# Kernel tuning notes

Hardware: AMD Instinct MI355X
Metric: run time of the kernel (lower is better)

Reference implementation:

```python
import jax, jax.numpy as jnp
import numpy as np
from jax import lax

R = 512          # num RoIs
K = 81           # num classes (COCO + bg)
IM_H, IM_W = 800, 1333
WX, WY, WW, WH = 10.0, 10.0, 5.0, 5.0   # cfg.MODEL.BBOX_REG_WEIGHTS
XFORM_CLIP = float(np.log(1000.0 / 16.0))  # cfg.BBOX_XFORM_CLIP
NMS_THRESH = 0.5
SCORE_THRESH = 0.001
MAX_PER_IMG = 100
POST_NMS_TOPN = 300


def setup_inputs() -> dict:
    key = jax.random.key(0)
    k1, k2, k3, k4, k5, k6 = jax.random.split(key, 6)
    # Build valid RoIs inside the image (x1<x2, y1<y2)
    cx = jax.random.uniform(k1, (R,)) * IM_W
    cy = jax.random.uniform(k2, (R,)) * IM_H
    w = jax.random.uniform(k3, (R,)) * 200.0 + 20.0
    h = jax.random.uniform(k4, (R,)) * 200.0 + 20.0
    rois = jnp.stack([
        jnp.clip(cx - 0.5 * w, 0.0, IM_W - 1),
        jnp.clip(cy - 0.5 * h, 0.0, IM_H - 1),
        jnp.clip(cx + 0.5 * w, 0.0, IM_W - 1),
        jnp.clip(cy + 0.5 * h, 0.0, IM_H - 1),
    ], axis=1).astype(jnp.float32)
    deltas = (jax.random.normal(k5, (R, 4 * K)) * 0.3).astype(jnp.float32)
    scores = jax.nn.softmax(jax.random.normal(k6, (R, K)) * 2.0, axis=1).astype(jnp.float32)
    return {"rois": rois, "deltas": deltas, "scores": scores}


def bbox_transform(boxes, deltas):
    # boxes [R,4], deltas [R,4K] -> pred boxes [R,K,4], clamped to image
    widths = boxes[:, 2] - boxes[:, 0] + 1.0
    heights = boxes[:, 3] - boxes[:, 1] + 1.0
    ctr_x = boxes[:, 0] + 0.5 * widths
    ctr_y = boxes[:, 1] + 0.5 * heights
    d = deltas.reshape(-1, K, 4)  # [R,K,4]
    dx = d[:, :, 0] / WX
    dy = d[:, :, 1] / WY
    dw = jnp.minimum(d[:, :, 2] / WW, XFORM_CLIP)
    dh = jnp.minimum(d[:, :, 3] / WH, XFORM_CLIP)
    pcx = dx * widths[:, None] + ctr_x[:, None]
    pcy = dy * heights[:, None] + ctr_y[:, None]
    pw = jnp.exp(dw) * widths[:, None]
    ph = jnp.exp(dh) * heights[:, None]
    x1 = jnp.clip(pcx - 0.5 * pw, 0.0, IM_W - 1)
    y1 = jnp.clip(pcy - 0.5 * ph, 0.0, IM_H - 1)
    x2 = jnp.clip(pcx + 0.5 * pw - 1.0, 0.0, IM_W - 1)
    y2 = jnp.clip(pcy + 0.5 * ph - 1.0, 0.0, IM_H - 1)
    return jnp.stack([x1, y1, x2, y2], axis=-1)  # [R,K,4]


def nms_one_class(scores_c, boxes_c):
    # Greedy NMS for one class. scores_c [R], boxes_c [R,4] -> keep mask [R] (orig order)
    order = jnp.argsort(-scores_c)
    b = boxes_c[order]
    areas = (b[:, 2] - b[:, 0] + 1.0) * (b[:, 3] - b[:, 1] + 1.0)
    xx1 = jnp.maximum(b[:, None, 0], b[None, :, 0])
    yy1 = jnp.maximum(b[:, None, 1], b[None, :, 1])
    xx2 = jnp.minimum(b[:, None, 2], b[None, :, 2])
    yy2 = jnp.minimum(b[:, None, 3], b[None, :, 3])
    inter = jnp.maximum(xx2 - xx1 + 1.0, 0.0) * jnp.maximum(yy2 - yy1 + 1.0, 0.0)
    iou = inter / (areas[:, None] + areas[None, :] - inter)
    suppress = iou > NMS_THRESH  # [R,R]
    idx = jnp.arange(R)

    def body(i, keep):
        sup = suppress[i] & keep[i] & (idx > i)
        return keep & (~sup)

    keep = lax.fori_loop(0, R, body, jnp.ones((R,), bool))
    keep = keep & (jnp.cumsum(keep) <= POST_NMS_TOPN)
    return jnp.zeros((R,), bool).at[order].set(keep)


def _detect(rois, deltas, scores):
    boxes3 = bbox_transform(rois, deltas)  # [R,K,4]
    # valid classes: max score over rois (excluding bg) above threshold
    cls_valid = jnp.concatenate([
        jnp.zeros((1,), bool),
        scores[:, 1:].max(axis=0) > SCORE_THRESH,
    ])  # [K]
    keep_kc = jax.vmap(nms_one_class, in_axes=(1, 1))(scores, boxes3)  # [K,R]
    nms_mask = (keep_kc.T & cls_valid[None, :]).astype(scores.dtype)  # [R,K]
    dists_all = nms_mask * scores
    # duplicate filtering: one label per box
    scores_pre = dists_all.max(axis=1)   # [R]
    labels_pre = dists_all.argmax(axis=1)
    order = jnp.argsort(-scores_pre)
    top = order[:MAX_PER_IMG]            # [100]
    scores_all = scores_pre[top]
    labels_all = labels_pre[top]
    valid = scores_all > SCORE_THRESH
    boxes_assign = boxes3.reshape(-1, 4)[top * K + labels_all]  # [100,4]
    scores_all = jnp.where(valid, scores_all, 0.0)
    boxes_assign = jnp.where(valid[:, None], boxes_assign, 0.0)
    out = jnp.concatenate([scores_all[:, None], boxes_assign], axis=1)  # [100,5]
    return out, labels_all, top


def reference(rois, deltas, scores):
    return _detect(rois, deltas, scores)
```

## Files before the change

kernel.cpp:

```cpp
#include <hip/hip_runtime.h>
#include <cstdint>
#include <cstddef>


#define R 512
#define K 81
#define IM_W_MAX 1332.0f
#define IM_H_MAX 799.0f
#define XFORM_CLIP_F 4.135166556742356f
#define NMS_THRESH_F 0.5f
#define SCORE_THRESH_F 0.001f
#define MAX_PER_IMG 100
#define POST_NMS_TOPN 300

__device__ __forceinline__ float4 transform_box(const float* __restrict__ rois,
                                                const float* __restrict__ deltas,
                                                int r, int k) {
    float4 roi = ((const float4*)rois)[r];
    float4 d4  = *(const float4*)(deltas + (size_t)r * (4 * K) + 4 * k);
    float w  = roi.z - roi.x + 1.0f;
    float h  = roi.w - roi.y + 1.0f;
    float cx = roi.x + 0.5f * w;
    float cy = roi.y + 0.5f * h;
    float dx = d4.x / 10.0f;
    float dy = d4.y / 10.0f;
    float dw = fminf(d4.z / 5.0f, XFORM_CLIP_F);
    float dh = fminf(d4.w / 5.0f, XFORM_CLIP_F);
    float pcx = dx * w + cx;
    float pcy = dy * h + cy;
    float pw  = expf(dw) * w;
    float ph  = expf(dh) * h;
    float4 b;
    b.x = fminf(fmaxf(pcx - 0.5f * pw, 0.0f), IM_W_MAX);
    b.y = fminf(fmaxf(pcy - 0.5f * ph, 0.0f), IM_H_MAX);
    b.z = fminf(fmaxf(pcx + 0.5f * pw - 1.0f, 0.0f), IM_W_MAX);
    b.w = fminf(fmaxf(pcy + 0.5f * ph - 1.0f, 0.0f), IM_H_MAX);
    return b;
}

__global__ void __launch_bounds__(512)
rank_boxes_kernel(const float* __restrict__ rois,
                  const float* __restrict__ deltas,
                  const float* __restrict__ scores,
                  float4* __restrict__ sbox_g,
                  int* __restrict__ order_g,
                  float* __restrict__ ssc_g,
                  int* __restrict__ valid_g) {
    const int k = blockIdx.x, tid = threadIdx.x;
    __shared__ unsigned long long s_key[R];
    __shared__ float s_red[R];

    const float sc = scores[tid * K + k];
    {
        unsigned int bits = __float_as_uint(sc);
        s_key[tid] = ((unsigned long long)(~bits) << 32) | (unsigned int)tid;
    }
    s_red[tid] = sc;
    __syncthreads();
    for (int s = 256; s > 0; s >>= 1) {
        if (tid < s) s_red[tid] = fmaxf(s_red[tid], s_red[tid + s]);
        __syncthreads();
    }
    const bool valid = (k != 0) && (s_red[0] > SCORE_THRESH_F);
    if (tid == 0) valid_g[k] = valid;
    if (!valid) return;

    const unsigned long long ki = s_key[tid];
    int cnt = 0;
    const ulonglong2* kp = (const ulonglong2*)s_key;
    #pragma unroll 8
    for (int j2 = 0; j2 < R / 2; ++j2) {
        ulonglong2 k2 = kp[j2];
        cnt += (k2.x < ki);
        cnt += (k2.y < ki);
    }
    sbox_g[k * R + cnt]  = transform_box(rois, deltas, tid, k);
    order_g[k * R + cnt] = tid;
    ssc_g[k * R + cnt]   = sc;
}

__global__ void __launch_bounds__(256)
bitmatrix_kernel(const float4* __restrict__ sbox_g,
                 const int* __restrict__ valid_g,
                 unsigned long long* __restrict__ supT_g) {
    const int b = blockIdx.x;
    const int k = b >> 3;
    const int w = b & 7;
    const int tid = threadIdx.x;
    if (!valid_g[k]) return;

    __shared__ float4 s_sbox[R];
    __shared__ float  s_area[R];
    for (int i = tid; i < R; i += 256) {
        float4 bx = sbox_g[k * R + i];
        s_sbox[i] = bx;
        s_area[i] = (bx.z - bx.x + 1.0f) * (bx.w - bx.y + 1.0f);
    }
    __syncthreads();

    const int jbase = w * 64;
    #pragma unroll
    for (int rep = 0; rep < 2; ++rep) {
        const int i = tid + rep * 256;
        const int d = i - jbase;
        unsigned long long mask =
            (d < 0) ? ~0ull : ((d >= 63) ? 0ull : (~0ull << (d + 1)));
        unsigned long long bits = 0ull;
        if (mask) {
            const float4 bi = s_sbox[i];
            const float  ai = s_area[i];
            #pragma unroll 8
            for (int jj = 0; jj < 64; ++jj) {
                float4 bj = s_sbox[jbase + jj];
                float  aj = s_area[jbase + jj];
                float xx1 = fmaxf(bi.x, bj.x);
                float yy1 = fmaxf(bi.y, bj.y);
                float xx2 = fminf(bi.z, bj.z);
                float yy2 = fminf(bi.w, bj.w);
                float iw = fmaxf(xx2 - xx1 + 1.0f, 0.0f);
                float ih = fmaxf(yy2 - yy1 + 1.0f, 0.0f);
                float inter = iw * ih;
                float iou = inter / (ai + aj - inter);
                bits |= (unsigned long long)(iou > NMS_THRESH_F) << jj;
            }
        }
        supT_g[k * 4096 + w * 512 + i] = bits & mask;
    }
}

__global__ void __launch_bounds__(64)
sweep_kernel(const unsigned long long* __restrict__ supT_g,
             const int* __restrict__ order_g,
             const float* __restrict__ ssc_g,
             const int* __restrict__ valid_g,
             float* __restrict__ dists_t) {
    const int k = blockIdx.x;
    const int l = threadIdx.x;

    if (!valid_g[k]) {
        #pragma unroll
        for (int p = 0; p < 8; ++p) dists_t[k * R + p * 64 + l] = 0.0f;
        return;
    }

    int   ord[8];
    float ssc[8];
    #pragma unroll
    for (int p = 0; p < 8; ++p) {
        ord[p] = order_g[k * R + p * 64 + l];
        ssc[p] = ssc_g[k * R + p * 64 + l];
    }

    const unsigned long long* base = supT_g + (size_t)k * 4096;
    unsigned long long rrow[8], rnext[8];
    #pragma unroll
    for (int w = 0; w < 8; ++w) rrow[w] = base[w * 512 + l];

    unsigned long long kb[8];
    #pragma unroll
    for (int w = 0; w < 8; ++w) kb[w] = ~0ull;

    #pragma unroll
    for (int wb = 0; wb < 8; ++wb) {
        if (wb < 7) {
            #pragma unroll
            for (int w = 0; w < 8; ++w)
                rnext[w] = (w > wb) ? base[w * 512 + (wb + 1) * 64 + l] : 0ull;
        }

        const unsigned long long nz = __ballot(rrow[wb] != 0ull);
        unsigned long long cur = kb[wb];
        unsigned long long m = cur & nz;
        while (m) {
            int bit = __builtin_ctzll(m);
            const unsigned int r_lo = (unsigned int)(rrow[wb] & 0xffffffffull);
            const unsigned int r_hi = (unsigned int)(rrow[wb] >> 32);
            unsigned long long row =
                ((unsigned long long)(unsigned int)__builtin_amdgcn_readlane((int)r_hi, bit) << 32) |
                 (unsigned long long)(unsigned int)__builtin_amdgcn_readlane((int)r_lo, bit);
            m &= m - 1;
            cur &= ~row;
            m   &= ~row;
        }
        kb[wb] = cur;

        #pragma unroll
        for (int w = wb + 1; w < 8; ++w) {
            unsigned long long contrib = ((cur >> l) & 1ull) ? rrow[w] : 0ull;
            if (__ballot(contrib != 0ull)) {
                #pragma unroll
                for (int off = 32; off > 0; off >>= 1)
                    contrib |= __shfl_xor(contrib, off, 64);
                kb[w] &= ~contrib;
            }
        }

        #pragma unroll
        for (int w = 0; w < 8; ++w) rrow[w] = rnext[w];
    }

    int total = 0;
    #pragma unroll
    for (int w = 0; w < 8; ++w) total += __popcll(kb[w]);
    if (total > POST_NMS_TOPN) {
        int cnt = 0;
        #pragma unroll
        for (int w = 0; w < 8; ++w) {
            int pc = __popcll(kb[w]);
            if (cnt + pc <= POST_NMS_TOPN) { cnt += pc; continue; }
            unsigned long long word = kb[w], outw = 0ull;
            int room = POST_NMS_TOPN - cnt;
            while (room > 0) {
                unsigned long long lsb = word & (~word + 1ull);
                outw |= lsb; word ^= lsb; --room;
            }
            kb[w] = outw; cnt = POST_NMS_TOPN;
        }
    }

    #pragma unroll
    for (int p = 0; p < 8; ++p)
        dists_t[k * R + ord[p]] = ((kb[p] >> l) & 1ull) ? ssc[p] : 0.0f;
}

__global__ void __launch_bounds__(512)
finalize_kernel(const float* __restrict__ dists_t,
                const float* __restrict__ rois,
                const float* __restrict__ deltas,
                float* __restrict__ out) {
    const int b = blockIdx.x;
    const int t = threadIdx.x;
    __shared__ unsigned long long s_key[R];
    __shared__ int s_arg[R];

    {
        const int r = t;
        float vmax = dists_t[r];
        int arg = 0;
        #pragma unroll 8
        for (int kk = 1; kk < K; ++kk) {
            float v = dists_t[kk * R + r];
            if (v > vmax) { vmax = v; arg = kk; }
        }
        unsigned int bits = __float_as_uint(vmax);
        s_key[r] = ((unsigned long long)(~bits) << 32) | (unsigned int)r;
        s_arg[r] = arg;
    }
    __syncthreads();

    const int ri = b * 64 + (t >> 3);
    const int c  = t & 7;
    const unsigned long long ki = s_key[ri];
    int cnt = 0;
    #pragma unroll 8
    for (int j = 0; j < 64; ++j) {
        int jj = (j + c * 8) & 63;
        cnt += (s_key[c * 64 + jj] < ki);
    }
    cnt += __shfl_xor(cnt, 1, 64);
    cnt += __shfl_xor(cnt, 2, 64);
    cnt += __shfl_xor(cnt, 4, 64);

    if (c == 0 && cnt < MAX_PER_IMG) {
        float vmax = __uint_as_float(~(unsigned int)(ki >> 32));
        int arg = s_arg[ri];
        bool valid = vmax > SCORE_THRESH_F;
        float4 bx = transform_box(rois, deltas, ri, arg);
        out[cnt * 5 + 0] = valid ? vmax : 0.0f;
        out[cnt * 5 + 1] = valid ? bx.x : 0.0f;
        out[cnt * 5 + 2] = valid ? bx.y : 0.0f;
        out[cnt * 5 + 3] = valid ? bx.z : 0.0f;
        out[cnt * 5 + 4] = valid ? bx.w : 0.0f;
        out[500 + cnt] = (float)arg;
        out[600 + cnt] = (float)ri;
    }
}

extern "C" void kernel_launch(void* const* d_in, const int* in_sizes, int n_in,
                              void* d_out, int out_size, void* d_ws, size_t ws_size,
                              hipStream_t stream) {
    const float* rois   = (const float*)d_in[0];
    const float* deltas = (const float*)d_in[1];
    const float* scores = (const float*)d_in[2];
    float* out = (float*)d_out;

    char* ws = (char*)d_ws;
    float4* sbox_g  = (float4*)(ws + 0);
    int*    order_g = (int*)   (ws + 663552);
    float*  ssc_g   = (float*) (ws + 829440);
    int*    valid_g = (int*)   (ws + 995328);
    float*  dists_t = (float*) (ws + 995840);
    unsigned long long* supT_g = (unsigned long long*)(ws + 1161728);

    rank_boxes_kernel<<<K, 512, 0, stream>>>(rois, deltas, scores,
                                             sbox_g, order_g, ssc_g, valid_g);
    bitmatrix_kernel <<<K * 8, 256, 0, stream>>>(sbox_g, valid_g, supT_g);
    sweep_kernel     <<<K, 64, 0, stream>>>(supT_g, order_g, ssc_g, valid_g, dists_t);
    finalize_kernel  <<<8, 512, 0, stream>>>(dists_t, rois, deltas, out);
}
```

Measured before the change: 111.3 us.

## Fuse ranking, IoU bitmatrix and sweep into one kernel with ticket election

```diff
diff --git a/kernel.cpp b/kernel.cpp
--- a/kernel.cpp
+++ b/kernel.cpp
@@ -38,134 +38,139 @@
     return b;
 }
 
-__global__ void __launch_bounds__(512)
-rank_boxes_kernel(const float* __restrict__ rois,
-                  const float* __restrict__ deltas,
-                  const float* __restrict__ scores,
-                  float4* __restrict__ sbox_g,
-                  int* __restrict__ order_g,
-                  float* __restrict__ ssc_g,
-                  int* __restrict__ valid_g) {
-    const int k = blockIdx.x, tid = threadIdx.x;
+__global__ void __launch_bounds__(256)
+nms_mega_kernel(const float* __restrict__ rois,
+                const float* __restrict__ deltas,
+                const float* __restrict__ scores,
+                unsigned long long* __restrict__ supT_g,
+                float* __restrict__ dists_t,
+                unsigned int* __restrict__ ticket) {
+    const int b   = blockIdx.x;
+    const int k   = b >> 3;
+    const int w   = b & 7;
+    const int tid = threadIdx.x;
+
     __shared__ unsigned long long s_key[R];
-    __shared__ float s_red[R];
-
-    const float sc = scores[tid * K + k];
+    __shared__ int    s_order[R];
+    __shared__ float  s_ssc[R];
+    __shared__ float4 s_sbox[R];
+    __shared__ float  s_area[R];
+    __shared__ float  s_red[256];
+    __shared__ int    s_winner;
+
+    const int i0 = tid, i1 = tid + 256;
+    const float sc0 = scores[i0 * K + k];
+    const float sc1 = scores[i1 * K + k];
     {
-        unsigned int bits = __float_as_uint(sc);
-        s_key[tid] = ((unsigned long long)(~bits) << 32) | (unsigned int)tid;
-    }
-    s_red[tid] = sc;
+        unsigned int b0 = __float_as_uint(sc0);
+        unsigned int b1 = __float_as_uint(sc1);
+        s_key[i0] = ((unsigned long long)(~b0) << 32) | (unsigned int)i0;
+        s_key[i1] = ((unsigned long long)(~b1) << 32) | (unsigned int)i1;
+    }
+    s_red[tid] = fmaxf(sc0, sc1);
     __syncthreads();
-    for (int s = 256; s > 0; s >>= 1) {
+    for (int s = 128; s > 0; s >>= 1) {
         if (tid < s) s_red[tid] = fmaxf(s_red[tid], s_red[tid + s]);
         __syncthreads();
     }
     const bool valid = (k != 0) && (s_red[0] > SCORE_THRESH_F);
-    if (tid == 0) valid_g[k] = valid;
-    if (!valid) return;
-
-    const unsigned long long ki = s_key[tid];
-    int cnt = 0;
-    const ulonglong2* kp = (const ulonglong2*)s_key;
-    #pragma unroll 8
-    for (int j2 = 0; j2 < R / 2; ++j2) {
-        ulonglong2 k2 = kp[j2];
-        cnt += (k2.x < ki);
-        cnt += (k2.y < ki);
-    }
-    sbox_g[k * R + cnt]  = transform_box(rois, deltas, tid, k);
-    order_g[k * R + cnt] = tid;
-    ssc_g[k * R + cnt]   = sc;
-}
-
-__global__ void __launch_bounds__(256)
-bitmatrix_kernel(const float4* __restrict__ sbox_g,
-                 const int* __restrict__ valid_g,
-                 unsigned long long* __restrict__ supT_g) {
-    const int b = blockIdx.x;
-    const int k = b >> 3;
-    const int w = b & 7;
-    const int tid = threadIdx.x;
-    if (!valid_g[k]) return;
-
-    __shared__ float4 s_sbox[R];
-    __shared__ float  s_area[R];
-    for (int i = tid; i < R; i += 256) {
-        float4 bx = sbox_g[k * R + i];
-        s_sbox[i] = bx;
-        s_area[i] = (bx.z - bx.x + 1.0f) * (bx.w - bx.y + 1.0f);
-    }
+
+    if (valid) {
+        {
+            const unsigned long long k0 = s_key[i0], k1 = s_key[i1];
+            int c0 = 0, c1 = 0;
+            const ulonglong2* kp = (const ulonglong2*)s_key;
+            #pragma unroll 8
+            for (int j2 = 0; j2 < R / 2; ++j2) {
+                ulonglong2 k2 = kp[j2];
+                c0 += (k2.x < k0); c0 += (k2.y < k0);
+                c1 += (k2.x < k1); c1 += (k2.y < k1);
+            }
+            s_order[c0] = i0; s_ssc[c0] = sc0;
+            s_order[c1] = i1; s_ssc[c1] = sc1;
+        }
+        __syncthreads();
+
+        #pragma unroll
+        for (int rep = 0; rep < 2; ++rep) {
+            const int rk = tid + rep * 256;
+            float4 bx = transform_box(rois, deltas, s_order[rk], k);
+            s_sbox[rk] = bx;
+            s_area[rk] = (bx.z - bx.x + 1.0f) * (bx.w - bx.y + 1.0f);
+        }
+        __syncthreads();
+
+        const int jbase = w * 64;
+        #pragma unroll
+        for (int rep = 0; rep < 2; ++rep) {
+            const int i = tid + rep * 256;
+            const int d = i - jbase;
+            unsigned long long mask =
+                (d < 0) ? ~0ull : ((d >= 63) ? 0ull : (~0ull << (d + 1)));
+            unsigned long long bits = 0ull;
+            if (mask) {
+                const float4 bi = s_sbox[i];
+                const float  ai = s_area[i];
+                #pragma unroll 8
+                for (int jj = 0; jj < 64; ++jj) {
+                    float4 bj = s_sbox[jbase + jj];
+                    float  aj = s_area[jbase + jj];
+                    float xx1 = fmaxf(bi.x, bj.x);
+                    float yy1 = fmaxf(bi.y, bj.y);
+                    float xx2 = fminf(bi.z, bj.z);
+                    float yy2 = fminf(bi.w, bj.w);
+                    float iw = fmaxf(xx2 - xx1 + 1.0f, 0.0f);
+                    float ih = fmaxf(yy2 - yy1 + 1.0f, 0.0f);
+                    float inter = iw * ih;
+                    float iou = inter / (ai + aj - inter);
+                    bits |= (unsigned long long)(iou > NMS_THRESH_F) << jj;
+                }
+            }
+            supT_g[k * 4096 + w * 512 + i] = bits & mask;
+        }
+    }
+
     __syncthreads();
-
-    const int jbase = w * 64;
-    #pragma unroll
-    for (int rep = 0; rep < 2; ++rep) {
-        const int i = tid + rep * 256;
-        const int d = i - jbase;
-        unsigned long long mask =
-            (d < 0) ? ~0ull : ((d >= 63) ? 0ull : (~0ull << (d + 1)));
-        unsigned long long bits = 0ull;
-        if (mask) {
-            const float4 bi = s_sbox[i];
-            const float  ai = s_area[i];
-            #pragma unroll 8
-            for (int jj = 0; jj < 64; ++jj) {
-                float4 bj = s_sbox[jbase + jj];
-                float  aj = s_area[jbase + jj];
-                float xx1 = fmaxf(bi.x, bj.x);
-                float yy1 = fmaxf(bi.y, bj.y);
-                float xx2 = fminf(bi.z, bj.z);
-                float yy2 = fminf(bi.w, bj.w);
-                float iw = fmaxf(xx2 - xx1 + 1.0f, 0.0f);
-                float ih = fmaxf(yy2 - yy1 + 1.0f, 0.0f);
-                float inter = iw * ih;
-                float iou = inter / (ai + aj - inter);
-                bits |= (unsigned long long)(iou > NMS_THRESH_F) << jj;
-            }
-        }
-        supT_g[k * 4096 + w * 512 + i] = bits & mask;
-    }
-}
-
-__global__ void __launch_bounds__(64)
-sweep_kernel(const unsigned long long* __restrict__ supT_g,
-             const int* __restrict__ order_g,
-             const float* __restrict__ ssc_g,
-             const int* __restrict__ valid_g,
-             float* __restrict__ dists_t) {
-    const int k = blockIdx.x;
-    const int l = threadIdx.x;
-
-    if (!valid_g[k]) {
-        #pragma unroll
-        for (int p = 0; p < 8; ++p) dists_t[k * R + p * 64 + l] = 0.0f;
+    if (tid == 0) {
+        __threadfence();
+        unsigned int t = atomicAdd(&ticket[k], 1u);
+        s_winner = (t == 7u);
+    }
+    __syncthreads();
+    if (!s_winner) return;
+    __threadfence();
+
+    if (!valid) {
+        #pragma unroll
+        for (int rep = 0; rep < 2; ++rep) dists_t[k * R + tid + rep * 256] = 0.0f;
         return;
     }
+    if (tid >= 64) return;
+    const int l = tid;
 
     int   ord[8];
     float ssc[8];
     #pragma unroll
     for (int p = 0; p < 8; ++p) {
-        ord[p] = order_g[k * R + p * 64 + l];
-        ssc[p] = ssc_g[k * R + p * 64 + l];
+        ord[p] = s_order[p * 64 + l];
+        ssc[p] = s_ssc[p * 64 + l];
     }
 
     const unsigned long long* base = supT_g + (size_t)k * 4096;
     unsigned long long rrow[8], rnext[8];
     #pragma unroll
-    for (int w = 0; w < 8; ++w) rrow[w] = base[w * 512 + l];
+    for (int ww = 0; ww < 8; ++ww) rrow[ww] = base[ww * 512 + l];
 
     unsigned long long kb[8];
     #pragma unroll
-    for (int w = 0; w < 8; ++w) kb[w] = ~0ull;
+    for (int ww = 0; ww < 8; ++ww) kb[ww] = ~0ull;
 
     #pragma unroll
     for (int wb = 0; wb < 8; ++wb) {
         if (wb < 7) {
             #pragma unroll
-            for (int w = 0; w < 8; ++w)
-                rnext[w] = (w > wb) ? base[w * 512 + (wb + 1) * 64 + l] : 0ull;
+            for (int ww = 0; ww < 8; ++ww)
+                rnext[ww] = (ww > wb) ? base[ww * 512 + (wb + 1) * 64 + l] : 0ull;
         }
 
         const unsigned long long nz = __ballot(rrow[wb] != 0ull);
@@ -185,36 +190,36 @@
         kb[wb] = cur;
 
         #pragma unroll
-        for (int w = wb + 1; w < 8; ++w) {
-            unsigned long long contrib = ((cur >> l) & 1ull) ? rrow[w] : 0ull;
+        for (int ww = wb + 1; ww < 8; ++ww) {
+            unsigned long long contrib = ((cur >> l) & 1ull) ? rrow[ww] : 0ull;
             if (__ballot(contrib != 0ull)) {
                 #pragma unroll
                 for (int off = 32; off > 0; off >>= 1)
                     contrib |= __shfl_xor(contrib, off, 64);
-                kb[w] &= ~contrib;
+                kb[ww] &= ~contrib;
             }
         }
 
         #pragma unroll
-        for (int w = 0; w < 8; ++w) rrow[w] = rnext[w];
+        for (int ww = 0; ww < 8; ++ww) rrow[ww] = rnext[ww];
     }
 
     int total = 0;
     #pragma unroll
-    for (int w = 0; w < 8; ++w) total += __popcll(kb[w]);
+    for (int ww = 0; ww < 8; ++ww) total += __popcll(kb[ww]);
     if (total > POST_NMS_TOPN) {
         int cnt = 0;
         #pragma unroll
-        for (int w = 0; w < 8; ++w) {
-            int pc = __popcll(kb[w]);
+        for (int ww = 0; ww < 8; ++ww) {
+            int pc = __popcll(kb[ww]);
             if (cnt + pc <= POST_NMS_TOPN) { cnt += pc; continue; }
-            unsigned long long word = kb[w], outw = 0ull;
+            unsigned long long word = kb[ww], outw = 0ull;
             int room = POST_NMS_TOPN - cnt;
             while (room > 0) {
                 unsigned long long lsb = word & (~word + 1ull);
                 outw |= lsb; word ^= lsb; --room;
             }
-            kb[w] = outw; cnt = POST_NMS_TOPN;
+            kb[ww] = outw; cnt = POST_NMS_TOPN;
         }
     }
 
@@ -285,16 +290,12 @@
     float* out = (float*)d_out;
 
     char* ws = (char*)d_ws;
-    float4* sbox_g  = (float4*)(ws + 0);
-    int*    order_g = (int*)   (ws + 663552);
-    float*  ssc_g   = (float*) (ws + 829440);
-    int*    valid_g = (int*)   (ws + 995328);
-    float*  dists_t = (float*) (ws + 995840);
-    unsigned long long* supT_g = (unsigned long long*)(ws + 1161728);
-
-    rank_boxes_kernel<<<K, 512, 0, stream>>>(rois, deltas, scores,
-                                             sbox_g, order_g, ssc_g, valid_g);
-    bitmatrix_kernel <<<K * 8, 256, 0, stream>>>(sbox_g, valid_g, supT_g);
-    sweep_kernel     <<<K, 64, 0, stream>>>(supT_g, order_g, ssc_g, valid_g, dists_t);
-    finalize_kernel  <<<8, 512, 0, stream>>>(dists_t, rois, deltas, out);
+    unsigned long long* supT_g = (unsigned long long*)(ws + 0);
+    float* dists_t = (float*)(ws + 2654208);
+    unsigned int* ticket = (unsigned int*)(ws + 2820096);
+
+    hipMemsetAsync(ticket, 0, K * sizeof(unsigned int), stream);
+    nms_mega_kernel<<<K * 8, 256, 0, stream>>>(rois, deltas, scores,
+                                               supT_g, dists_t, ticket);
+    finalize_kernel<<<8, 512, 0, stream>>>(dists_t, rois, deltas, out);
 }
```

Result: slower. 152.5 us (+37.0%).

## Fuse sweep and finalize via atomic counter, split ranking across blocks, fast IoU test

Applied to the files above, without the earlier changes.

```diff
diff --git a/kernel.cpp b/kernel.cpp
--- a/kernel.cpp
+++ b/kernel.cpp
@@ -38,34 +38,44 @@
     return b;
 }
 
-__global__ void __launch_bounds__(512)
+__global__ void __launch_bounds__(128)
 rank_boxes_kernel(const float* __restrict__ rois,
                   const float* __restrict__ deltas,
                   const float* __restrict__ scores,
                   float4* __restrict__ sbox_g,
                   int* __restrict__ order_g,
                   float* __restrict__ ssc_g,
-                  int* __restrict__ valid_g) {
-    const int k = blockIdx.x, tid = threadIdx.x;
+                  int* __restrict__ valid_g,
+                  unsigned int* __restrict__ done) {
+    const int b = blockIdx.x;
+    const int k = b >> 2, q = b & 3;
+    const int tid = threadIdx.x;
     __shared__ unsigned long long s_key[R];
-    __shared__ float s_red[R];
-
-    const float sc = scores[tid * K + k];
-    {
+    __shared__ float s_red[128];
+
+    if (b == 0 && tid == 0) *done = 0u;
+
+    float m = -1.0f;
+    #pragma unroll
+    for (int p = 0; p < 4; ++p) {
+        const int i = p * 128 + tid;
+        float sc = scores[i * K + k];
         unsigned int bits = __float_as_uint(sc);
-        s_key[tid] = ((unsigned long long)(~bits) << 32) | (unsigned int)tid;
-    }
-    s_red[tid] = sc;
+        s_key[i] = ((unsigned long long)(~bits) << 32) | (unsigned int)i;
+        m = fmaxf(m, sc);
+    }
+    s_red[tid] = m;
     __syncthreads();
-    for (int s = 256; s > 0; s >>= 1) {
+    for (int s = 64; s > 0; s >>= 1) {
         if (tid < s) s_red[tid] = fmaxf(s_red[tid], s_red[tid + s]);
         __syncthreads();
     }
     const bool valid = (k != 0) && (s_red[0] > SCORE_THRESH_F);
-    if (tid == 0) valid_g[k] = valid;
+    if (q == 0 && tid == 0) valid_g[k] = valid;
     if (!valid) return;
 
-    const unsigned long long ki = s_key[tid];
+    const int ri = q * 128 + tid;
+    const unsigned long long ki = s_key[ri];
     int cnt = 0;
     const ulonglong2* kp = (const ulonglong2*)s_key;
     #pragma unroll 8
@@ -74,9 +84,9 @@
         cnt += (k2.x < ki);
         cnt += (k2.y < ki);
     }
-    sbox_g[k * R + cnt]  = transform_box(rois, deltas, tid, k);
-    order_g[k * R + cnt] = tid;
-    ssc_g[k * R + cnt]   = sc;
+    sbox_g[k * R + cnt]  = transform_box(rois, deltas, ri, k);
+    order_g[k * R + cnt] = ri;
+    ssc_g[k * R + cnt]   = __uint_as_float(~(unsigned int)(ki >> 32));
 }
 
 __global__ void __launch_bounds__(256)
@@ -120,121 +130,140 @@
                 float iw = fmaxf(xx2 - xx1 + 1.0f, 0.0f);
                 float ih = fmaxf(yy2 - yy1 + 1.0f, 0.0f);
                 float inter = iw * ih;
-                float iou = inter / (ai + aj - inter);
-                bits |= (unsigned long long)(iou > NMS_THRESH_F) << jj;
+                float denom = ai + aj - inter;
+                float two_i = inter + inter;
+                float hi = denom * 1.0000002f;
+                float lo = denom * 0.99999976f;
+                bool sup = two_i > hi;
+                if (!sup && !(two_i < lo)) {
+                    sup = (inter / denom) > NMS_THRESH_F;
+                }
+                bits |= (unsigned long long)sup << jj;
             }
         }
         supT_g[k * 4096 + w * 512 + i] = bits & mask;
     }
 }
 
-__global__ void __launch_bounds__(64)
-sweep_kernel(const unsigned long long* __restrict__ supT_g,
-             const int* __restrict__ order_g,
-             const float* __restrict__ ssc_g,
-             const int* __restrict__ valid_g,
-             float* __restrict__ dists_t) {
-    const int k = blockIdx.x;
-    const int l = threadIdx.x;
-
-    if (!valid_g[k]) {
-        #pragma unroll
-        for (int p = 0; p < 8; ++p) dists_t[k * R + p * 64 + l] = 0.0f;
+__global__ void __launch_bounds__(256)
+sweep_finalize_kernel(const unsigned long long* __restrict__ supT_g,
+                      const int* __restrict__ order_g,
+                      const float* __restrict__ ssc_g,
+                      const int* __restrict__ valid_g,
+                      const float* __restrict__ rois,
+                      const float* __restrict__ deltas,
+                      float* __restrict__ dists_t,
+                      unsigned int* __restrict__ done,
+                      float* __restrict__ out) {
+    const int b   = blockIdx.x;
+    const int tid = threadIdx.x;
+
+    if (b < K) {
+        if (tid >= 64) return;
+        const int k = b, l = tid;
+
+        if (valid_g[k]) {
+            int   ord[8];
+            float ssc[8];
+            #pragma unroll
+            for (int p = 0; p < 8; ++p) {
+                ord[p] = order_g[k * R + p * 64 + l];
+                ssc[p] = ssc_g[k * R + p * 64 + l];
+            }
+
+            const unsigned long long* base = supT_g + (size_t)k * 4096;
+            unsigned long long rrow[8], rnext[8];
+            #pragma unroll
+            for (int ww = 0; ww < 8; ++ww) rrow[ww] = base[ww * 512 + l];
+
+            unsigned long long kb[8];
+            #pragma unroll
+            for (int ww = 0; ww < 8; ++ww) kb[ww] = ~0ull;
+
+            #pragma unroll
+            for (int wb = 0; wb < 8; ++wb) {
+                if (wb < 7) {
+                    #pragma unroll
+                    for (int ww = 0; ww < 8; ++ww)
+                        rnext[ww] = (ww > wb) ? base[ww * 512 + (wb + 1) * 64 + l] : 0ull;
+                }
+                const unsigned long long nz = __ballot(rrow[wb] != 0ull);
+                unsigned long long cur = kb[wb];
+                unsigned long long m = cur & nz;
+                while (m) {
+                    int bit = __builtin_ctzll(m);
+                    const unsigned int r_lo = (unsigned int)(rrow[wb] & 0xffffffffull);
+                    const unsigned int r_hi = (unsigned int)(rrow[wb] >> 32);
+                    unsigned long long row =
+                        ((unsigned long long)(unsigned int)__builtin_amdgcn_readlane((int)r_hi, bit) << 32) |
+                         (unsigned long long)(unsigned int)__builtin_amdgcn_readlane((int)r_lo, bit);
+                    m &= m - 1;
+                    cur &= ~row;
+                    m   &= ~row;
+                }
+                kb[wb] = cur;
+
+                #pragma unroll
+                for (int ww = wb + 1; ww < 8; ++ww) {
+                    unsigned long long contrib = ((cur >> l) & 1ull) ? rrow[ww] : 0ull;
+                    if (__ballot(contrib != 0ull)) {
+                        #pragma unroll
+                        for (int off = 32; off > 0; off >>= 1)
+                            contrib |= __shfl_xor(contrib, off, 64);
+                        kb[ww] &= ~contrib;
+                    }
+                }
+                #pragma unroll
+                for (int ww = 0; ww < 8; ++ww) rrow[ww] = rnext[ww];
+            }
+
+            int total = 0;
+            #pragma unroll
+            for (int ww = 0; ww < 8; ++ww) total += __popcll(kb[ww]);
+            if (total > POST_NMS_TOPN) {
+                int cnt = 0;
+                #pragma unroll
+                for (int ww = 0; ww < 8; ++ww) {
+                    int pc = __popcll(kb[ww]);
+                    if (cnt + pc <= POST_NMS_TOPN) { cnt += pc; continue; }
+                    unsigned long long word = kb[ww], outw = 0ull;
+                    int room = POST_NMS_TOPN - cnt;
+                    while (room > 0) {
+                        unsigned long long lsb = word & (~word + 1ull);
+                        outw |= lsb; word ^= lsb; --room;
+                    }
+                    kb[ww] = outw; cnt = POST_NMS_TOPN;
+                }
+            }
+            #pragma unroll
+            for (int p = 0; p < 8; ++p)
+                dists_t[k * R + ord[p]] = ((kb[p] >> l) & 1ull) ? ssc[p] : 0.0f;
+        } else {
+            #pragma unroll
+            for (int p = 0; p < 8; ++p) dists_t[k * R + p * 64 + l] = 0.0f;
+        }
+
+        if (l == 0) {
+            __threadfence();
+            atomicAdd(done, 1u);
+        }
         return;
     }
 
-    int   ord[8];
-    float ssc[8];
-    #pragma unroll
-    for (int p = 0; p < 8; ++p) {
-        ord[p] = order_g[k * R + p * 64 + l];
-        ssc[p] = ssc_g[k * R + p * 64 + l];
-    }
-
-    const unsigned long long* base = supT_g + (size_t)k * 4096;
-    unsigned long long rrow[8], rnext[8];
-    #pragma unroll
-    for (int w = 0; w < 8; ++w) rrow[w] = base[w * 512 + l];
-
-    unsigned long long kb[8];
-    #pragma unroll
-    for (int w = 0; w < 8; ++w) kb[w] = ~0ull;
-
-    #pragma unroll
-    for (int wb = 0; wb < 8; ++wb) {
-        if (wb < 7) {
-            #pragma unroll
-            for (int w = 0; w < 8; ++w)
-                rnext[w] = (w > wb) ? base[w * 512 + (wb + 1) * 64 + l] : 0ull;
-        }
-
-        const unsigned long long nz = __ballot(rrow[wb] != 0ull);
-        unsigned long long cur = kb[wb];
-        unsigned long long m = cur & nz;
-        while (m) {
-            int bit = __builtin_ctzll(m);
-            const unsigned int r_lo = (unsigned int)(rrow[wb] & 0xffffffffull);
-            const unsigned int r_hi = (unsigned int)(rrow[wb] >> 32);
-            unsigned long long row =
-                ((unsigned long long)(unsigned int)__builtin_amdgcn_readlane((int)r_hi, bit) << 32) |
-                 (unsigned long long)(unsigned int)__builtin_amdgcn_readlane((int)r_lo, bit);
-            m &= m - 1;
-            cur &= ~row;
-            m   &= ~row;
-        }
-        kb[wb] = cur;
-
-        #pragma unroll
-        for (int w = wb + 1; w < 8; ++w) {
-            unsigned long long contrib = ((cur >> l) & 1ull) ? rrow[w] : 0ull;
-            if (__ballot(contrib != 0ull)) {
-                #pragma unroll
-                for (int off = 32; off > 0; off >>= 1)
-                    contrib |= __shfl_xor(contrib, off, 64);
-                kb[w] &= ~contrib;
-            }
-        }
-
-        #pragma unroll
-        for (int w = 0; w < 8; ++w) rrow[w] = rnext[w];
-    }
-
-    int total = 0;
-    #pragma unroll
-    for (int w = 0; w < 8; ++w) total += __popcll(kb[w]);
-    if (total > POST_NMS_TOPN) {
-        int cnt = 0;
-        #pragma unroll
-        for (int w = 0; w < 8; ++w) {
-            int pc = __popcll(kb[w]);
-            if (cnt + pc <= POST_NMS_TOPN) { cnt += pc; continue; }
-            unsigned long long word = kb[w], outw = 0ull;
-            int room = POST_NMS_TOPN - cnt;
-            while (room > 0) {
-                unsigned long long lsb = word & (~word + 1ull);
-                outw |= lsb; word ^= lsb; --room;
-            }
-            kb[w] = outw; cnt = POST_NMS_TOPN;
-        }
-    }
-
-    #pragma unroll
-    for (int p = 0; p < 8; ++p)
-        dists_t[k * R + ord[p]] = ((kb[p] >> l) & 1ull) ? ssc[p] : 0.0f;
-}
-
-__global__ void __launch_bounds__(512)
-finalize_kernel(const float* __restrict__ dists_t,
-                const float* __restrict__ rois,
-                const float* __restrict__ deltas,
-                float* __restrict__ out) {
-    const int b = blockIdx.x;
-    const int t = threadIdx.x;
     __shared__ unsigned long long s_key[R];
     __shared__ int s_arg[R];
-
-    {
-        const int r = t;
+    const int fb = b - K;
+
+    if (tid == 0) {
+        while (__hip_atomic_load(done, __ATOMIC_ACQUIRE,
+                                 __HIP_MEMORY_SCOPE_AGENT) < (unsigned)K)
+            __builtin_amdgcn_s_sleep(8);
+    }
+    __syncthreads();
+
+    #pragma unroll
+    for (int rep = 0; rep < 2; ++rep) {
+        const int r = tid + rep * 256;
         float vmax = dists_t[r];
         int arg = 0;
         #pragma unroll 8
@@ -248,18 +277,15 @@
     }
     __syncthreads();
 
-    const int ri = b * 64 + (t >> 3);
-    const int c  = t & 7;
+    const int ri = fb * 64 + (tid >> 2);
+    const int c  = tid & 3;
     const unsigned long long ki = s_key[ri];
     int cnt = 0;
     #pragma unroll 8
-    for (int j = 0; j < 64; ++j) {
-        int jj = (j + c * 8) & 63;
-        cnt += (s_key[c * 64 + jj] < ki);
-    }
+    for (int j = 0; j < 128; ++j)
+        cnt += (s_key[c * 128 + j] < ki);
     cnt += __shfl_xor(cnt, 1, 64);
     cnt += __shfl_xor(cnt, 2, 64);
-    cnt += __shfl_xor(cnt, 4, 64);
 
     if (c == 0 && cnt < MAX_PER_IMG) {
         float vmax = __uint_as_float(~(unsigned int)(ki >> 32));
@@ -291,10 +317,13 @@
     int*    valid_g = (int*)   (ws + 995328);
     float*  dists_t = (float*) (ws + 995840);
     unsigned long long* supT_g = (unsigned long long*)(ws + 1161728);
-
-    rank_boxes_kernel<<<K, 512, 0, stream>>>(rois, deltas, scores,
-                                             sbox_g, order_g, ssc_g, valid_g);
-    bitmatrix_kernel <<<K * 8, 256, 0, stream>>>(sbox_g, valid_g, supT_g);
-    sweep_kernel     <<<K, 64, 0, stream>>>(supT_g, order_g, ssc_g, valid_g, dists_t);
-    finalize_kernel  <<<8, 512, 0, stream>>>(dists_t, rois, deltas, out);
-}
+    unsigned int* done = (unsigned int*)(ws + 3815936);
+
+    rank_boxes_kernel    <<<K * 4, 128, 0, stream>>>(rois, deltas, scores,
+                                                     sbox_g, order_g, ssc_g,
+                                                     valid_g, done);
+    bitmatrix_kernel     <<<K * 8, 256, 0, stream>>>(sbox_g, valid_g, supT_g);
+    sweep_finalize_kernel<<<K + 8, 256, 0, stream>>>(supT_g, order_g, ssc_g,
+                                                     valid_g, rois, deltas,
+                                                     dists_t, done, out);
+}
```

New measurement: 115.7 us. +3.9%, slower.
